# Optimization experiments

Measured on AMD Instinct MI355X. Metric: run time of the kernel, lower is better.

The kernel has to match this reference:

```python
import jax, jax.numpy as jnp
import numpy as np

N = 1024      # layer_size (power of 2)
B = 16384     # batch
DEPTH = 2     # Butterfly depth (default)


def _abcd_offsets(n):
    """Factor sizes n, n/2, ..., 2 and their offsets into the packed ABCD buffer.
    A factor of size m has ABCD of shape (2, 2, m//2, 2) = 2m complex pairs."""
    offs = []
    off = 0
    m = n
    while m >= 2:
        offs.append((m, off))
        off += 2 * m
        m //= 2
    return offs, off  # off == 4n - 4


def setup_inputs() -> dict:
    key = jax.random.key(0)
    k1, k2, k3 = jax.random.split(key, 3)
    _, total = _abcd_offsets(N)
    x = jax.random.normal(k1, (B, N), jnp.float32)
    perm_logit = jax.random.normal(k2, (DEPTH, 3), jnp.float32)
    # scale ~1/sqrt(2) so the product of log2(n) random 2x2 blocks stays bounded
    abcd = jax.random.normal(k3, (DEPTH, total, 2), jnp.float32) * 0.7
    b = jnp.zeros((N,), jnp.float32)
    return {"x": x, "perm_logit": perm_logit, "abcd": abcd, "b": b}


def _perm_factor(h, p, m):
    """One BlockPerm factor (soft permutation) of size m applied blockwise.
    h: (B, n, 2) real/imag pairs. p: (3,) probabilities.
    p[0]: mix with even/odd separation; p[1], p[2]: mix each half with its reversal."""
    Bn, n, _ = h.shape
    h = h.reshape(Bn, n // m, m, 2)
    eo = jnp.concatenate([h[:, :, 0::2], h[:, :, 1::2]], axis=2)
    h = (1 - p[0]) * h + p[0] * eo
    h1, h2 = h[:, :, : m // 2], h[:, :, m // 2 :]
    h1 = (1 - p[1]) * h1 + p[1] * h1[:, :, ::-1]
    h2 = (1 - p[2]) * h2 + p[2] * h2[:, :, ::-1]
    return jnp.concatenate([h1, h2], axis=2).reshape(Bn, n, 2)


def _diag_factor(h, ABCD, m):
    """One Block2x2Diag factor of size m: out = [[A,B],[C,D]] x with diagonal A,B,C,D.
    h: (B, n, 2); ABCD: (2, 2, m//2, 2) complex pairs."""
    Bn, n, _ = h.shape
    hv = h.reshape(Bn, n // m, 2, m // 2, 2)  # (B, blocks, halves, m/2, cplx)
    xr, xi = hv[..., 0], hv[..., 1]
    Ar, Ai = ABCD[..., 0], ABCD[..., 1]
    yr = jnp.einsum('ijk,bnjk->bnik', Ar, xr) - jnp.einsum('ijk,bnjk->bnik', Ai, xi)
    yi = jnp.einsum('ijk,bnjk->bnik', Ar, xi) + jnp.einsum('ijk,bnjk->bnik', Ai, xr)
    return jnp.stack([yr, yi], axis=-1).reshape(Bn, n, 2)


def _forward(x, perm_logit, abcd, b):
    n = x.shape[-1]
    offs, _ = _abcd_offsets(n)
    # real_to_complex: (B, n) -> (B, n, 2)
    h = jnp.stack([x, jnp.zeros_like(x)], axis=-1)
    perm_sizes = [m for (m, _) in offs if m >= 4]
    depth = perm_logit.shape[0]
    for d in range(depth):
        # BlockPermProduct (share_logit=True): all factors share one (3,) logit
        p = jax.nn.sigmoid(perm_logit[d])
        for m in reversed(perm_sizes):      # smallest factor first
            h = _perm_factor(h, p, m)
        # Block2x2DiagProduct: factors applied smallest size first
        for (m, off) in reversed(offs):
            ABCD = abcd[d, off:off + 2 * m].reshape(2, 2, m // 2, 2)
            h = _diag_factor(h, ABCD, m)
    out = h[..., 0]  # take real part
    return b + out


def reference(x, perm_logit, abcd, b):
    return _forward(x, perm_logit, abcd, b)
```

## Files before the change

kernel.cpp:

```cpp
#include <hip/hip_runtime.h>
#include <hip/hip_bf16.h>
#include <stdint.h>

#define N_DIM 1024
#define DEPTH 2
#define ABCD_TOTAL 4092

typedef __attribute__((ext_vector_type(8))) short short8;
typedef __attribute__((ext_vector_type(4))) float floatx4;
typedef __attribute__((ext_vector_type(4))) float f4;

__device__ __forceinline__ f4 cmul(float cr, float ci, f4 v) {
    f4 r;
    r[0] = cr * v[0] - ci * v[1];
    r[1] = cr * v[1] + ci * v[0];
    r[2] = cr * v[2] - ci * v[3];
    r[3] = cr * v[3] + ci * v[2];
    return r;
}

__global__ __launch_bounds__(256) void build_and_cast(
    const float* __restrict__ perm_logit,
    const float* __restrict__ abcd,
    const float* __restrict__ x,
    __hip_bfloat16* __restrict__ S,
    __hip_bfloat16* __restrict__ xb)
{
    const int bx  = blockIdx.x;
    const int tid = threadIdx.x;
    __shared__ f4 h[2][N_DIM];

    if (bx >= 512) {
        const int cb = bx - 512;
        const size_t i = ((size_t)cb * 256 + tid) * 8;
        float4 v0 = *(const float4*)(x + i);
        float4 v1 = *(const float4*)(x + i + 4);
        union { __hip_bfloat16 e[8]; int4 v; } u;
        u.e[0] = __float2bfloat16(v0.x); u.e[1] = __float2bfloat16(v0.y);
        u.e[2] = __float2bfloat16(v0.z); u.e[3] = __float2bfloat16(v0.w);
        u.e[4] = __float2bfloat16(v1.x); u.e[5] = __float2bfloat16(v1.y);
        u.e[6] = __float2bfloat16(v1.z); u.e[7] = __float2bfloat16(v1.w);
        *(int4*)(xb + i) = u.v;
        return;
    }

    const int row0 = bx * 2;
    const f4 zz = {0.0f, 0.0f, 0.0f, 0.0f};
    for (int j = tid; j < N_DIM; j += 256) { h[0][j] = zz; h[1][j] = zz; }
    __syncthreads();
    if (tid == 0) {
        f4 e0 = {1.0f, 0.0f, 0.0f, 0.0f};
        f4 e1 = {0.0f, 0.0f, 1.0f, 0.0f};
        h[0][row0]     = e0;
        h[0][row0 + 1] = e1;
    }
    __syncthreads();

    int cur = 0;
    for (int d = 0; d < DEPTH; ++d) {
        const float p0 = 1.0f / (1.0f + expf(-perm_logit[d * 3 + 0]));
        const float p1 = 1.0f / (1.0f + expf(-perm_logit[d * 3 + 1]));
        const float p2 = 1.0f / (1.0f + expf(-perm_logit[d * 3 + 2]));

#pragma unroll
        for (int s = 2; s <= 10; ++s) {
            const int half = 1 << (s - 1), hq = half >> 1;
            const int cnt   = (d == 0) ? half : 512;
            const int pbase = (d == 0) ? ((row0 >> s) << (s - 1)) : 0;
            const f4* __restrict__ in = h[cur];
            f4* __restrict__ out      = h[cur ^ 1];
            for (int tt = tid; tt < cnt; tt += 256) {
                const int t    = pbase + tt;
                const int blk  = t >> (s - 1);
                const int r    = t & (half - 1);
                const int base = blk << s;
                int q1, q2; float pc;
                if (r < hq) { q1 = r;           q2 = half - 1 - r;   pc = p1; }
                else        { int r2 = r - hq;  q1 = half + r2;
                              q2 = 2 * half - 1 - r2;                pc = p2; }
                const int src1 = (q1 < half) ? 2 * q1 : 2 * (q1 - half) + 1;
                const int src2 = (q2 < half) ? 2 * q2 : 2 * (q2 - half) + 1;
                f4 b1 = in[base + q1], a1 = in[base + src1];
                f4 b2 = in[base + q2], a2 = in[base + src2];
                f4 s1a = b1 + p0 * (a1 - b1);
                f4 s1b = b2 + p0 * (a2 - b2);
                out[base + q1] = s1a + pc * (s1b - s1a);
                out[base + q2] = s1b + pc * (s1a - s1b);
            }
            __syncthreads();
            cur ^= 1;
        }

        const float* __restrict__ abd = abcd + (size_t)d * (ABCD_TOTAL * 2);
#pragma unroll
        for (int s = 1; s <= 9; s += 2) {
            const int hh = 1 << (s - 1);
            const float* __restrict__ ab1 = abd + (size_t)(4096 - 8 * hh) * 2;
            const float* __restrict__ ab2 = abd + (size_t)(4096 - 16 * hh) * 2;
            const f4* __restrict__ in = h[cur];
            f4* __restrict__ out      = h[cur ^ 1];
            {
                const int g     = tid;
                const int k     = g & (hh - 1);
                const int base2 = (g >> (s - 1)) << (s + 1);
                f4 x0 = in[base2 + k];
                f4 x1 = in[base2 + k + hh];
                f4 x2 = in[base2 + k + 2 * hh];
                f4 x3 = in[base2 + k + 3 * hh];
                float2 A = *(const float2*)(ab1 + 2 * (size_t)k);
                float2 B = *(const float2*)(ab1 + 2 * (size_t)(hh + k));
                float2 C = *(const float2*)(ab1 + 2 * (size_t)(2 * hh + k));
                float2 D = *(const float2*)(ab1 + 2 * (size_t)(3 * hh + k));
                f4 y0 = cmul(A.x, A.y, x0) + cmul(B.x, B.y, x1);
                f4 y1 = cmul(C.x, C.y, x0) + cmul(D.x, D.y, x1);
                f4 y2 = cmul(A.x, A.y, x2) + cmul(B.x, B.y, x3);
                f4 y3 = cmul(C.x, C.y, x2) + cmul(D.x, D.y, x3);
                float2 A2 = *(const float2*)(ab2 + 2 * (size_t)k);
                float2 B2 = *(const float2*)(ab2 + 2 * (size_t)(2 * hh + k));
                float2 C2 = *(const float2*)(ab2 + 2 * (size_t)(4 * hh + k));
                float2 D2 = *(const float2*)(ab2 + 2 * (size_t)(6 * hh + k));
                float2 A3 = *(const float2*)(ab2 + 2 * (size_t)(hh + k));
                float2 B3 = *(const float2*)(ab2 + 2 * (size_t)(3 * hh + k));
                float2 C3 = *(const float2*)(ab2 + 2 * (size_t)(5 * hh + k));
                float2 D3 = *(const float2*)(ab2 + 2 * (size_t)(7 * hh + k));
                out[base2 + k]          = cmul(A2.x, A2.y, y0) + cmul(B2.x, B2.y, y2);
                out[base2 + k + 2 * hh] = cmul(C2.x, C2.y, y0) + cmul(D2.x, D2.y, y2);
                out[base2 + k + hh]     = cmul(A3.x, A3.y, y1) + cmul(B3.x, B3.y, y3);
                out[base2 + k + 3 * hh] = cmul(C3.x, C3.y, y1) + cmul(D3.x, D3.y, y3);
            }
            __syncthreads();
            cur ^= 1;
        }
    }

    for (int j = tid; j < N_DIM; j += 256) {
        f4 v = h[cur][j];
        S[(size_t)row0 * N_DIM + j]       = __float2bfloat16(v[0]);
        S[(size_t)(row0 + 1) * N_DIM + j] = __float2bfloat16(v[2]);
    }
}

__global__ __launch_bounds__(256) void transpose_w(
    const __hip_bfloat16* __restrict__ S, __hip_bfloat16* __restrict__ Wt)
{
    const int i0 = (blockIdx.x & 15) * 64;
    const int j0 = (blockIdx.x >> 4) * 64;
    __shared__ __hip_bfloat16 tile[64][72];
    const int r  = threadIdx.x >> 2;
    const int c0 = (threadIdx.x & 3) * 16;
    *(short8*)&tile[r][c0]     = *(const short8*)(S + (size_t)(i0 + r) * N_DIM + j0 + c0);
    *(short8*)&tile[r][c0 + 8] = *(const short8*)(S + (size_t)(i0 + r) * N_DIM + j0 + c0 + 8);
    __syncthreads();
    union { __hip_bfloat16 e[8]; short8 v; } o1, o2;
#pragma unroll
    for (int k = 0; k < 8; ++k) { o1.e[k] = tile[c0 + k][r]; o2.e[k] = tile[c0 + 8 + k][r]; }
    *(short8*)(Wt + (size_t)(j0 + r) * N_DIM + i0 + c0)     = o1.v;
    *(short8*)(Wt + (size_t)(j0 + r) * N_DIM + i0 + c0 + 8) = o2.v;
}

#define BM 128
#define BN 128
#define BK 32

__device__ __forceinline__ void gl_lds16(const void* g, void* l) {
    __builtin_amdgcn_global_load_lds(
        (const __attribute__((address_space(1))) uint32_t*)g,
        (__attribute__((address_space(3))) uint32_t*)l, 16, 0, 0);
}

__global__ __launch_bounds__(256) void gemm_bt(
    const __hip_bfloat16* __restrict__ A,
    const __hip_bfloat16* __restrict__ Bt,
    const float* __restrict__ bias,
    float* __restrict__ C)
{
    const int tid = threadIdx.x;
    const int bx  = blockIdx.x;
    const int xcd = bx & 7;
    const int loc = bx >> 3;
    const int m0  = (xcd * 16 + (loc >> 3)) * BM;
    const int n0  = (loc & 7) * BN;

    __shared__ __hip_bfloat16 sA[BM * BK];
    __shared__ __hip_bfloat16 sB[BN * BK];

    const int lane = tid & 63;
    const int wm   = ((tid >> 6) & 1) * 64;
    const int wn   = ((tid >> 6) >> 1) * 64;
    const int lrow = lane & 15;
    const int lq   = lane >> 4;

    const int r1  = tid >> 2;
    const int c1s = (tid & 3) ^ ((tid >> 3) & 3);
    const int swz = (lrow >> 1) & 3;
    const int ca  = lq ^ swz;

    floatx4 acc[4][4] = {};

    for (int kt = 0; kt < 32; ++kt) {
        const int k0 = kt * BK;
        gl_lds16(A  + (size_t)(m0 + r1)      * N_DIM + k0 + c1s * 8, (char*)sA + tid * 16);
        gl_lds16(A  + (size_t)(m0 + 64 + r1) * N_DIM + k0 + c1s * 8, (char*)sA + (tid + 256) * 16);
        gl_lds16(Bt + (size_t)(n0 + r1)      * N_DIM + k0 + c1s * 8, (char*)sB + tid * 16);
        gl_lds16(Bt + (size_t)(n0 + 64 + r1) * N_DIM + k0 + c1s * 8, (char*)sB + (tid + 256) * 16);
        __syncthreads();

        short8 af[4], bf[4];
#pragma unroll
        for (int i = 0; i < 4; ++i) {
            af[i] = *(const short8*)((const char*)sA + ((wm + i * 16 + lrow) * 4 + ca) * 16);
            bf[i] = *(const short8*)((const char*)sB + ((wn + i * 16 + lrow) * 4 + ca) * 16);
        }
#pragma unroll
        for (int i = 0; i < 4; ++i)
#pragma unroll
            for (int j = 0; j < 4; ++j)
                acc[i][j] = __builtin_amdgcn_mfma_f32_16x16x32_bf16(
                    af[i], bf[j], acc[i][j], 0, 0, 0);
        __syncthreads();
    }

#pragma unroll
    for (int j = 0; j < 4; ++j) {
        const int gn = n0 + wn + j * 16 + lrow;
        const float bv = bias[gn];
#pragma unroll
        for (int i = 0; i < 4; ++i) {
            const int gm = m0 + wm + i * 16 + lq * 4;
#pragma unroll
            for (int r = 0; r < 4; ++r)
                C[(size_t)(gm + r) * N_DIM + gn] = acc[i][j][r] + bv;
        }
    }
}

extern "C" void kernel_launch(void* const* d_in, const int* in_sizes, int n_in,
                              void* d_out, int out_size, void* d_ws, size_t ws_size,
                              hipStream_t stream) {
    const float* x          = (const float*)d_in[0];
    const float* perm_logit = (const float*)d_in[1];
    const float* abcd       = (const float*)d_in[2];
    const float* bias       = (const float*)d_in[3];
    float* out              = (float*)d_out;

    __hip_bfloat16* S  = (__hip_bfloat16*)d_out;
    __hip_bfloat16* Wt = (__hip_bfloat16*)d_ws;
    __hip_bfloat16* xb = (__hip_bfloat16*)((char*)d_ws + (1 << 21));

    build_and_cast<<<dim3(512 + 8192), dim3(256), 0, stream>>>(perm_logit, abcd, x, S, xb);
    transpose_w<<<dim3(256), dim3(256), 0, stream>>>(S, Wt);
    gemm_bt<<<dim3(1024), dim3(256), 0, stream>>>(xb, Wt, bias, out);
}
```

Before: 164.8 us.

## Use wave barriers for intra-wave butterfly stages and widen GEMM K tile

```diff
diff --git a/kernel.cpp b/kernel.cpp
--- a/kernel.cpp
+++ b/kernel.cpp
@@ -64,6 +64,8 @@
 
 #pragma unroll
         for (int s = 2; s <= 10; ++s) {
+            if (s >= 8) __syncthreads();
+            else        __builtin_amdgcn_wave_barrier();
             const int half = 1 << (s - 1), hq = half >> 1;
             const int cnt   = (d == 0) ? half : 512;
             const int pbase = (d == 0) ? ((row0 >> s) << (s - 1)) : 0;
@@ -87,13 +89,15 @@
                 out[base + q1] = s1a + pc * (s1b - s1a);
                 out[base + q2] = s1b + pc * (s1a - s1b);
             }
-            __syncthreads();
             cur ^= 1;
         }
+        __syncthreads();
 
         const float* __restrict__ abd = abcd + (size_t)d * (ABCD_TOTAL * 2);
 #pragma unroll
         for (int s = 1; s <= 9; s += 2) {
+            if (s == 9) __syncthreads();
+            else        __builtin_amdgcn_wave_barrier();
             const int hh = 1 << (s - 1);
             const float* __restrict__ ab1 = abd + (size_t)(4096 - 8 * hh) * 2;
             const float* __restrict__ ab2 = abd + (size_t)(4096 - 16 * hh) * 2;
@@ -128,9 +132,9 @@
                 out[base2 + k + hh]     = cmul(A3.x, A3.y, y1) + cmul(B3.x, B3.y, y3);
                 out[base2 + k + 3 * hh] = cmul(C3.x, C3.y, y1) + cmul(D3.x, D3.y, y3);
             }
-            __syncthreads();
             cur ^= 1;
         }
+        __syncthreads();
     }
 
     for (int j = tid; j < N_DIM; j += 256) {
@@ -160,7 +164,7 @@
 
 #define BM 128
 #define BN 128
-#define BK 32
+#define BK 64
 
 __device__ __forceinline__ void gl_lds16(const void* g, void* l) {
     __builtin_amdgcn_global_load_lds(
@@ -168,7 +172,7 @@
         (__attribute__((address_space(3))) uint32_t*)l, 16, 0, 0);
 }
 
-__global__ __launch_bounds__(256) void gemm_bt(
+__global__ __launch_bounds__(256, 4) void gemm_bt(
     const __hip_bfloat16* __restrict__ A,
     const __hip_bfloat16* __restrict__ Bt,
     const float* __restrict__ bias,
@@ -190,33 +194,40 @@
     const int lrow = lane & 15;
     const int lq   = lane >> 4;
 
-    const int r1  = tid >> 2;
-    const int c1s = (tid & 3) ^ ((tid >> 3) & 3);
-    const int swz = (lrow >> 1) & 3;
-    const int ca  = lq ^ swz;
+    const int r1 = tid >> 3;
+    const int cs = (tid & 7) ^ (r1 & 7);
+    const int swz = lrow & 7;
 
     floatx4 acc[4][4] = {};
 
-    for (int kt = 0; kt < 32; ++kt) {
+    for (int kt = 0; kt < 16; ++kt) {
         const int k0 = kt * BK;
-        gl_lds16(A  + (size_t)(m0 + r1)      * N_DIM + k0 + c1s * 8, (char*)sA + tid * 16);
-        gl_lds16(A  + (size_t)(m0 + 64 + r1) * N_DIM + k0 + c1s * 8, (char*)sA + (tid + 256) * 16);
-        gl_lds16(Bt + (size_t)(n0 + r1)      * N_DIM + k0 + c1s * 8, (char*)sB + tid * 16);
-        gl_lds16(Bt + (size_t)(n0 + 64 + r1) * N_DIM + k0 + c1s * 8, (char*)sB + (tid + 256) * 16);
-        __syncthreads();
-
-        short8 af[4], bf[4];
-#pragma unroll
-        for (int i = 0; i < 4; ++i) {
-            af[i] = *(const short8*)((const char*)sA + ((wm + i * 16 + lrow) * 4 + ca) * 16);
-            bf[i] = *(const short8*)((const char*)sB + ((wn + i * 16 + lrow) * 4 + ca) * 16);
-        }
 #pragma unroll
         for (int i = 0; i < 4; ++i)
-#pragma unroll
-            for (int j = 0; j < 4; ++j)
-                acc[i][j] = __builtin_amdgcn_mfma_f32_16x16x32_bf16(
-                    af[i], bf[j], acc[i][j], 0, 0, 0);
+            gl_lds16(A + (size_t)(m0 + r1 + i * 32) * N_DIM + k0 + cs * 8,
+                     (char*)sA + (tid + i * 256) * 16);
+#pragma unroll
+        for (int i = 0; i < 4; ++i)
+            gl_lds16(Bt + (size_t)(n0 + r1 + i * 32) * N_DIM + k0 + cs * 8,
+                     (char*)sB + (tid + i * 256) * 16);
+        __syncthreads();
+
+#pragma unroll
+        for (int ks = 0; ks < 2; ++ks) {
+            short8 af[4], bf[4];
+            const int cc = (lq + 4 * ks) ^ swz;
+#pragma unroll
+            for (int i = 0; i < 4; ++i) {
+                af[i] = *(const short8*)((const char*)sA + (((wm + i * 16 + lrow) * 8 + cc) * 16));
+                bf[i] = *(const short8*)((const char*)sB + (((wn + i * 16 + lrow) * 8 + cc) * 16));
+            }
+#pragma unroll
+            for (int i = 0; i < 4; ++i)
+#pragma unroll
+                for (int j = 0; j < 4; ++j)
+                    acc[i][j] = __builtin_amdgcn_mfma_f32_16x16x32_bf16(
+                        af[i], bf[j], acc[i][j], 0, 0, 0);
+        }
         __syncthreads();
     }
 
```

Result: faster. 155.9 us (-5.4%).
